# Optimization experiments

Hardware: AMD Instinct MI355X
Metric: run time of the kernel (lower is better)

The kernel has to match this reference:

```python
import jax, jax.numpy as jnp
import numpy as np

N = 100000   # nodes
E = 3200000  # edges (avg degree 32)
D = 128      # node_input_dim
H = 32       # hidden_dim
OUT = 3


def setup_inputs() -> dict:
    key = jax.random.key(0)
    ks = jax.random.split(key, 8)
    x = jax.random.normal(ks[0], (N, D), jnp.float32)
    edge_index = jax.random.randint(ks[1], (2, E), 0, N, dtype=jnp.int32)
    W1 = jax.random.normal(ks[2], (D, H), jnp.float32) * (1.0 / np.sqrt(D))
    b1 = jnp.zeros((H,), jnp.float32)
    W2 = jax.random.normal(ks[3], (H, H), jnp.float32) * (1.0 / np.sqrt(H))
    b2 = jnp.zeros((H,), jnp.float32)
    Wfc = jax.random.normal(ks[4], (H, OUT), jnp.float32) * (1.0 / np.sqrt(H))
    bfc = jnp.zeros((OUT,), jnp.float32)
    return {"x": x, "edge_index": edge_index, "W1": W1, "b1": b1,
            "W2": W2, "b2": b2, "Wfc": Wfc, "bfc": bfc}


def gcn_conv(x, W, b, src, dst, num_nodes):
    # PyG GCNConv defaults: transform, add self-loops, symmetric deg^-1/2 norm, bias.
    h = x @ W  # [N, H]
    ones = jnp.ones(src.shape[0], x.dtype)
    # degree with self-loop (+1), counted at target index (col) as in PyG
    deg = jax.ops.segment_sum(ones, dst, num_segments=num_nodes) + 1.0
    norm = jax.lax.rsqrt(deg)  # [N]
    coef = norm[src] * norm[dst]  # [E]
    msg = h[src] * coef[:, None]  # [E, H] gather + scale
    agg = jax.ops.segment_sum(msg, dst, num_segments=num_nodes)  # scatter-add
    # self-loop contribution: norm[i]^2 * h[i]
    agg = agg + h * (norm * norm)[:, None]
    return agg + b


def reference(x, edge_index, W1, b1, W2, b2, Wfc, bfc):
    src, dst = edge_index[0], edge_index[1]
    n = x.shape[0]
    h = jax.nn.relu(gcn_conv(x, W1, b1, src, dst, n))
    h = jax.nn.relu(gcn_conv(h, W2, b2, src, dst, n))
    return jax.nn.sigmoid(h @ Wfc + bfc)
```

## Files before the change

kernel.cpp:

```cpp
#include <hip/hip_runtime.h>
#include <hip/hip_fp16.h>
#include <math.h>

#define D_IN   128
#define H_DIM  32
#define OUT_DIM 3

#define BS      256
#define LOGBS   8
#define CAP_B   9088
#define EPB_P   8192
#define NB_MAX  1024

static __device__ inline unsigned int h2u(__half2 h) {
    union { __half2 h; unsigned int u; } c; c.h = h; return c.u;
}
static __device__ inline __half2 u2h(unsigned int u) {
    union { unsigned int u; __half2 h; } c; c.u = u; return c.h;
}
static __device__ inline __half2 sh2(__half2 v, int o) {
    return u2h((unsigned int)__shfl_xor((int)h2u(v), o));
}


__global__ void k_init_cur(int* bcur, int nb) {
    int i = blockIdx.x * blockDim.x + threadIdx.x;
    if (i < nb) bcur[i] = i * CAP_B;
}


__global__ __launch_bounds__(256) void k_part(
    const int* __restrict__ src, const int* __restrict__ dst,
    int* __restrict__ bcur, int* __restrict__ tmcsr, int e, int nb)
{
    __shared__ int hist[NB_MAX];
    __shared__ int cur[NB_MAX];
    const int t = threadIdx.x;
    for (int j = t; j < nb; j += 256) hist[j] = 0;
    __syncthreads();

    const int base = blockIdx.x * EPB_P;
    int d[EPB_P / 256], s[EPB_P / 256];
#pragma unroll
    for (int k = 0; k < EPB_P / 256; ++k) {
        int i = base + k * 256 + t;
        if (i < e) {
            d[k] = dst[i];
            s[k] = src[i];
            atomicAdd(&hist[d[k] >> LOGBS], 1);
        } else d[k] = -1;
    }
    __syncthreads();
    for (int j = t; j < nb; j += 256)
        cur[j] = hist[j] ? atomicAdd(&bcur[j], hist[j]) : 0;
    __syncthreads();
#pragma unroll
    for (int k = 0; k < EPB_P / 256; ++k) {
        if (d[k] >= 0) {
            int b = d[k] >> LOGBS;
            int pos = atomicAdd(&cur[b], 1);
            if (pos < (b + 1) * CAP_B)
                tmcsr[pos] = s[k] | ((d[k] & (BS - 1)) << 17);
        }
    }
}


__global__ __launch_bounds__(256) void k_build(
    int* __restrict__ tmcsr, const int* __restrict__ bcur,
    int* __restrict__ offs, int* __restrict__ ends, float* __restrict__ norm,
    int n)
{
    __shared__ int cnt[BS];
    __shared__ int ss[256];
    __shared__ int slice[CAP_B];

    const int t = threadIdx.x;
    const int b = blockIdx.x;
    const int bo = b * CAP_B;
    int m = bcur[b] - bo;
    if (m > CAP_B) m = CAP_B;

    cnt[t] = 0;
    __syncthreads();

    for (int i = t; i < m; i += 256)
        atomicAdd(&cnt[tmcsr[bo + i] >> 17], 1);
    __syncthreads();

    int c0 = cnt[t];
    ss[t] = c0;
    __syncthreads();
    for (int off = 1; off < 256; off <<= 1) {
        int u = (t >= off) ? ss[t - off] : 0;
        __syncthreads();
        ss[t] += u;
        __syncthreads();
    }
    int eb = ss[t] - c0;

    int node = (b << LOGBS) + t;
    if (node < n) {
        offs[node] = bo + eb;
        ends[node] = bo + eb + c0;
        norm[node] = rsqrtf((float)c0 + 1.0f);
    }
    cnt[t] = eb;
    __syncthreads();

    for (int i = t; i < m; i += 256) {
        int p = tmcsr[bo + i];
        int pos = atomicAdd(&cnt[p >> 17], 1);
        if (pos < CAP_B) slice[pos] = p & 0x1FFFF;
    }
    __syncthreads();

    for (int i = t; i < m; i += 256) tmcsr[bo + i] = slice[i];
}


__global__ __launch_bounds__(256) void k_gemm1(
    const float* __restrict__ x, const float* __restrict__ W1,
    const float* __restrict__ norm, __half* __restrict__ h1s, int n)
{
    __shared__ float Wl[D_IN * H_DIM];
    for (int i = threadIdx.x; i < D_IN * H_DIM; i += 256) Wl[i] = W1[i];
    __syncthreads();

    const int t = threadIdx.x;
    const int jg = t & 3;
    const int node = blockIdx.x * 64 + (t >> 2);
    if (node >= n) return;
    const int j0 = jg * 8;

    float acc[8];
#pragma unroll
    for (int j = 0; j < 8; ++j) acc[j] = 0.0f;

    const float* xrow = &x[(size_t)node * D_IN];
    for (int k = 0; k < D_IN; k += 4) {
        const float4 xv = *(const float4*)&xrow[k];
#pragma unroll
        for (int kk = 0; kk < 4; ++kk) {
            const float xs = (kk == 0) ? xv.x : (kk == 1) ? xv.y
                           : (kk == 2) ? xv.z : xv.w;
            const float4 wa = *(const float4*)&Wl[(k + kk) * H_DIM + j0];
            const float4 wb = *(const float4*)&Wl[(k + kk) * H_DIM + j0 + 4];
            acc[0] = fmaf(xs, wa.x, acc[0]);
            acc[1] = fmaf(xs, wa.y, acc[1]);
            acc[2] = fmaf(xs, wa.z, acc[2]);
            acc[3] = fmaf(xs, wa.w, acc[3]);
            acc[4] = fmaf(xs, wb.x, acc[4]);
            acc[5] = fmaf(xs, wb.y, acc[5]);
            acc[6] = fmaf(xs, wb.z, acc[6]);
            acc[7] = fmaf(xs, wb.w, acc[7]);
        }
    }

    const float nr = norm[node];
    uint4 pk;
    pk.x = h2u(__floats2half2_rn(acc[0]*nr, acc[1]*nr));
    pk.y = h2u(__floats2half2_rn(acc[2]*nr, acc[3]*nr));
    pk.z = h2u(__floats2half2_rn(acc[4]*nr, acc[5]*nr));
    pk.w = h2u(__floats2half2_rn(acc[6]*nr, acc[7]*nr));
    *(uint4*)&h1s[(size_t)node * H_DIM + j0] = pk;
}


__global__ __launch_bounds__(256) void k_gather_g2(
    const __half* __restrict__ hsA, const float* __restrict__ norm,
    const int* __restrict__ offs, const int* __restrict__ ends,
    const int* __restrict__ csr, const float* __restrict__ b1,
    const float* __restrict__ W2, __half* __restrict__ hsB, int n)
{
    __shared__ float Wl[H_DIM * 33];
    __shared__ float bl[H_DIM];
    for (int i = threadIdx.x; i < H_DIM * H_DIM; i += 256) {
        int k = i >> 5, j = i & 31;
        Wl[k * 33 + j] = W2[i];
    }
    if (threadIdx.x < H_DIM) bl[threadIdx.x] = b1[threadIdx.x];
    __syncthreads();

    const int t = threadIdx.x;
    const int node = blockIdx.x * 4 + (t >> 6);
    if (node >= n) return;
    const int lane = t & 63;
    const int g = lane >> 3;
    const int q = lane & 7;

    const int beg = offs[node];
    const int end = ends[node];
    const uint2* rows = (const uint2*)hsA;

    uint2 rs = rows[node * 8 + q];

    __half2 acc0 = u2h(0u), acc1 = u2h(0u);
    int j = beg + g;
    for (; j + 24 < end; j += 32) {
        int s0 = csr[j];
        int s1 = csr[j + 8];
        int s2 = csr[j + 16];
        int s3 = csr[j + 24];
        uint2 r0 = rows[s0 * 8 + q];
        uint2 r1 = rows[s1 * 8 + q];
        uint2 r2 = rows[s2 * 8 + q];
        uint2 r3 = rows[s3 * 8 + q];
        acc0 = __hadd2(acc0, __hadd2(__hadd2(u2h(r0.x), u2h(r1.x)),
                                     __hadd2(u2h(r2.x), u2h(r3.x))));
        acc1 = __hadd2(acc1, __hadd2(__hadd2(u2h(r0.y), u2h(r1.y)),
                                     __hadd2(u2h(r2.y), u2h(r3.y))));
    }
    for (; j < end; j += 8) {
        uint2 r0 = rows[csr[j] * 8 + q];
        acc0 = __hadd2(acc0, u2h(r0.x));
        acc1 = __hadd2(acc1, u2h(r0.y));
    }
    if (g == 0) {
        acc0 = __hadd2(acc0, u2h(rs.x));
        acc1 = __hadd2(acc1, u2h(rs.y));
    }

#pragma unroll
    for (int o = 8; o < 64; o <<= 1) {
        acc0 = __hadd2(acc0, sh2(acc0, o));
        acc1 = __hadd2(acc1, sh2(acc1, o));
    }

    const float nr = norm[node];
    float2 f0 = __half22float2(acc0);
    float2 f1 = __half22float2(acc1);
    const int kb = q * 4;
    float u0 = fmaxf(fmaf(f0.x, nr, bl[kb + 0]), 0.f);
    float u1 = fmaxf(fmaf(f0.y, nr, bl[kb + 1]), 0.f);
    float u2 = fmaxf(fmaf(f1.x, nr, bl[kb + 2]), 0.f);
    float u3 = fmaxf(fmaf(f1.y, nr, bl[kb + 3]), 0.f);

    float p[4];
#pragma unroll
    for (int jj = 0; jj < 4; ++jj) {
        int jc = g + 8 * jj;
        p[jj] = u0 * Wl[(kb + 0) * 33 + jc]
              + u1 * Wl[(kb + 1) * 33 + jc]
              + u2 * Wl[(kb + 2) * 33 + jc]
              + u3 * Wl[(kb + 3) * 33 + jc];
    }
#pragma unroll
    for (int o = 1; o < 8; o <<= 1) {
        p[0] += __shfl_xor(p[0], o); p[1] += __shfl_xor(p[1], o);
        p[2] += __shfl_xor(p[2], o); p[3] += __shfl_xor(p[3], o);
    }

    if (q == 0) {
        __half* rowB = &hsB[(size_t)node * H_DIM];
        rowB[g]      = __float2half(p[0] * nr);
        rowB[g + 8]  = __float2half(p[1] * nr);
        rowB[g + 16] = __float2half(p[2] * nr);
        rowB[g + 24] = __float2half(p[3] * nr);
    }
}


__global__ __launch_bounds__(256) void k_gather_fin(
    const __half* __restrict__ hs, const float* __restrict__ norm,
    const int* __restrict__ offs, const int* __restrict__ ends,
    const int* __restrict__ csr, const float* __restrict__ b2,
    const float* __restrict__ Wfc, const float* __restrict__ bfc,
    float* __restrict__ out, int n)
{
    const int t = threadIdx.x;
    const int node = blockIdx.x * 4 + (t >> 6);
    if (node >= n) return;
    const int lane = t & 63;
    const int g = lane >> 3;
    const int q = lane & 7;

    const int beg = offs[node];
    const int end = ends[node];
    const uint2* rows = (const uint2*)hs;

    uint2 rs = rows[node * 8 + q];

    __half2 acc0 = u2h(0u), acc1 = u2h(0u);
    int j = beg + g;
    for (; j + 24 < end; j += 32) {
        int s0 = csr[j];
        int s1 = csr[j + 8];
        int s2 = csr[j + 16];
        int s3 = csr[j + 24];
        uint2 r0 = rows[s0 * 8 + q];
        uint2 r1 = rows[s1 * 8 + q];
        uint2 r2 = rows[s2 * 8 + q];
        uint2 r3 = rows[s3 * 8 + q];
        acc0 = __hadd2(acc0, __hadd2(__hadd2(u2h(r0.x), u2h(r1.x)),
                                     __hadd2(u2h(r2.x), u2h(r3.x))));
        acc1 = __hadd2(acc1, __hadd2(__hadd2(u2h(r0.y), u2h(r1.y)),
                                     __hadd2(u2h(r2.y), u2h(r3.y))));
    }
    for (; j < end; j += 8) {
        uint2 r0 = rows[csr[j] * 8 + q];
        acc0 = __hadd2(acc0, u2h(r0.x));
        acc1 = __hadd2(acc1, u2h(r0.y));
    }
    if (g == 0) {
        acc0 = __hadd2(acc0, u2h(rs.x));
        acc1 = __hadd2(acc1, u2h(rs.y));
    }

#pragma unroll
    for (int o = 8; o < 64; o <<= 1) {
        acc0 = __hadd2(acc0, sh2(acc0, o));
        acc1 = __hadd2(acc1, sh2(acc1, o));
    }

    const float nr = norm[node];
    float2 f0 = __half22float2(acc0);
    float2 f1 = __half22float2(acc1);
    const int f = q * 4;
    float v0 = fmaxf(fmaf(f0.x, nr, b2[f + 0]), 0.f);
    float v1 = fmaxf(fmaf(f0.y, nr, b2[f + 1]), 0.f);
    float v2 = fmaxf(fmaf(f1.x, nr, b2[f + 2]), 0.f);
    float v3 = fmaxf(fmaf(f1.y, nr, b2[f + 3]), 0.f);
    float p0 = v0*Wfc[(f+0)*3+0] + v1*Wfc[(f+1)*3+0] + v2*Wfc[(f+2)*3+0] + v3*Wfc[(f+3)*3+0];
    float p1 = v0*Wfc[(f+0)*3+1] + v1*Wfc[(f+1)*3+1] + v2*Wfc[(f+2)*3+1] + v3*Wfc[(f+3)*3+1];
    float p2 = v0*Wfc[(f+0)*3+2] + v1*Wfc[(f+1)*3+2] + v2*Wfc[(f+2)*3+2] + v3*Wfc[(f+3)*3+2];
#pragma unroll
    for (int o = 1; o < 8; o <<= 1) {
        p0 += __shfl_xor(p0, o); p1 += __shfl_xor(p1, o); p2 += __shfl_xor(p2, o);
    }

    if (lane == 0) {
        out[(size_t)node * 3 + 0] = 1.0f / (1.0f + expf(-(p0 + bfc[0])));
        out[(size_t)node * 3 + 1] = 1.0f / (1.0f + expf(-(p1 + bfc[1])));
        out[(size_t)node * 3 + 2] = 1.0f / (1.0f + expf(-(p2 + bfc[2])));
    }
}


extern "C" void kernel_launch(void* const* d_in, const int* in_sizes, int n_in,
                              void* d_out, int out_size, void* d_ws, size_t ws_size,
                              hipStream_t stream)
{
    const float* x   = (const float*)d_in[0];
    const int*   ei  = (const int*)d_in[1];
    const float* W1  = (const float*)d_in[2];
    const float* b1  = (const float*)d_in[3];
    const float* W2  = (const float*)d_in[4];
    const float* b2  = (const float*)d_in[5];
    const float* Wfc = (const float*)d_in[6];
    const float* bfc = (const float*)d_in[7];
    float* out = (float*)d_out;

    const int n = in_sizes[0] / D_IN;
    const int e = in_sizes[1] / 2;
    const int* src = ei;
    const int* dst = ei + e;
    const int nb = (n + BS - 1) >> LOGBS;

    size_t nAl = ((size_t)n + 256) & ~(size_t)255;

    float* norm  = (float*)d_ws;
    int*   offs  = (int*)(norm + nAl);
    int*   ends  = offs + nAl;
    int*   bcur  = ends + nAl;
    int*   tmcsr = bcur + 1024;
    __half* HbA  = (__half*)(tmcsr + (size_t)nb * CAP_B);
    __half* HbB  = HbA + nAl * H_DIM;

    const int nb_gm = (n + 63) / 64;
    const int nb_p  = (e + EPB_P - 1) / EPB_P;
    const int nb_g  = (n + 3) / 4;

    k_init_cur<<<(nb + 255) / 256, 256, 0, stream>>>(bcur, nb);
    k_part <<<nb_p, 256, 0, stream>>>(src, dst, bcur, tmcsr, e, nb);
    k_build<<<nb, 256, 0, stream>>>(tmcsr, bcur, offs, ends, norm, n);

    k_gemm1<<<nb_gm, 256, 0, stream>>>(x, W1, norm, HbA, n);

    k_gather_g2<<<nb_g, 256, 0, stream>>>(HbA, norm, offs, ends, tmcsr,
                                          b1, W2, HbB, n);

    k_gather_fin<<<nb_g, 256, 0, stream>>>(HbB, norm, offs, ends, tmcsr,
                                           b2, Wfc, bfc, out, n);
}
```

Before: 208.8 us.

## Enlarge block sizes for partition, build, and GEMM kernels; coalesce layer-2 stores

Partitioning now uses 512 threads per block and handles 16384 edges per block. Bucket cursors become relative offsets, so the init kernel is replaced by a memset. The build and first-layer GEMM kernels move to 512 threads, with the GEMM covering 128 nodes per block. The layer-2 gather stages its outputs in shared memory and writes each half-precision row with 8-byte vector stores instead of scattered 2-byte writes. The aim is fewer launches, fewer partition blocks contending on global atomics, and more coalesced writes. In exchange, register pressure in the partition kernel rises, and the build kernel leaves half its threads idle during the scan.

```diff
diff --git a/kernel.cpp b/kernel.cpp
--- a/kernel.cpp
+++ b/kernel.cpp
@@ -9,7 +9,9 @@
 #define BS      256
 #define LOGBS   8
 #define CAP_B   9088
-#define EPB_P   8192
+#define TPB_P   512
+#define EPB_P   16384
+#define VPT_P   (EPB_P / TPB_P)
 #define NB_MAX  1024
 
 static __device__ inline unsigned int h2u(__half2 h) {
@@ -23,27 +25,21 @@
 }
 
 
-__global__ void k_init_cur(int* bcur, int nb) {
-    int i = blockIdx.x * blockDim.x + threadIdx.x;
-    if (i < nb) bcur[i] = i * CAP_B;
-}
-
-
-__global__ __launch_bounds__(256) void k_part(
+__global__ __launch_bounds__(TPB_P) void k_part(
     const int* __restrict__ src, const int* __restrict__ dst,
     int* __restrict__ bcur, int* __restrict__ tmcsr, int e, int nb)
 {
     __shared__ int hist[NB_MAX];
     __shared__ int cur[NB_MAX];
     const int t = threadIdx.x;
-    for (int j = t; j < nb; j += 256) hist[j] = 0;
+    for (int j = t; j < nb; j += TPB_P) hist[j] = 0;
     __syncthreads();
 
     const int base = blockIdx.x * EPB_P;
-    int d[EPB_P / 256], s[EPB_P / 256];
-#pragma unroll
-    for (int k = 0; k < EPB_P / 256; ++k) {
-        int i = base + k * 256 + t;
+    int d[VPT_P], s[VPT_P];
+#pragma unroll
+    for (int k = 0; k < VPT_P; ++k) {
+        int i = base + k * TPB_P + t;
         if (i < e) {
             d[k] = dst[i];
             s[k] = src[i];
@@ -51,85 +47,87 @@
         } else d[k] = -1;
     }
     __syncthreads();
-    for (int j = t; j < nb; j += 256)
+    for (int j = t; j < nb; j += TPB_P)
         cur[j] = hist[j] ? atomicAdd(&bcur[j], hist[j]) : 0;
     __syncthreads();
 #pragma unroll
-    for (int k = 0; k < EPB_P / 256; ++k) {
+    for (int k = 0; k < VPT_P; ++k) {
         if (d[k] >= 0) {
             int b = d[k] >> LOGBS;
             int pos = atomicAdd(&cur[b], 1);
-            if (pos < (b + 1) * CAP_B)
-                tmcsr[pos] = s[k] | ((d[k] & (BS - 1)) << 17);
+            if (pos < CAP_B)
+                tmcsr[b * CAP_B + pos] = s[k] | ((d[k] & (BS - 1)) << 17);
         }
     }
 }
 
 
-__global__ __launch_bounds__(256) void k_build(
+__global__ __launch_bounds__(512) void k_build(
     int* __restrict__ tmcsr, const int* __restrict__ bcur,
     int* __restrict__ offs, int* __restrict__ ends, float* __restrict__ norm,
     int n)
 {
     __shared__ int cnt[BS];
-    __shared__ int ss[256];
+    __shared__ int ss[BS];
     __shared__ int slice[CAP_B];
 
     const int t = threadIdx.x;
     const int b = blockIdx.x;
     const int bo = b * CAP_B;
-    int m = bcur[b] - bo;
+    int m = bcur[b];
     if (m > CAP_B) m = CAP_B;
 
-    cnt[t] = 0;
-    __syncthreads();
-
-    for (int i = t; i < m; i += 256)
+    if (t < BS) cnt[t] = 0;
+    __syncthreads();
+
+    for (int i = t; i < m; i += 512)
         atomicAdd(&cnt[tmcsr[bo + i] >> 17], 1);
     __syncthreads();
 
-    int c0 = cnt[t];
-    ss[t] = c0;
-    __syncthreads();
-    for (int off = 1; off < 256; off <<= 1) {
-        int u = (t >= off) ? ss[t - off] : 0;
+    int c0 = 0;
+    if (t < BS) { c0 = cnt[t]; ss[t] = c0; }
+    __syncthreads();
+    for (int off = 1; off < BS; off <<= 1) {
+        int u = 0;
+        if (t < BS && t >= off) u = ss[t - off];
         __syncthreads();
-        ss[t] += u;
+        if (t < BS) ss[t] += u;
         __syncthreads();
     }
-    int eb = ss[t] - c0;
-
-    int node = (b << LOGBS) + t;
-    if (node < n) {
-        offs[node] = bo + eb;
-        ends[node] = bo + eb + c0;
-        norm[node] = rsqrtf((float)c0 + 1.0f);
-    }
-    cnt[t] = eb;
-    __syncthreads();
-
-    for (int i = t; i < m; i += 256) {
+    if (t < BS) {
+        int eb = ss[t] - c0;
+        int node = (b << LOGBS) + t;
+        if (node < n) {
+            offs[node] = bo + eb;
+            ends[node] = bo + eb + c0;
+            norm[node] = rsqrtf((float)c0 + 1.0f);
+        }
+        cnt[t] = eb;
+    }
+    __syncthreads();
+
+    for (int i = t; i < m; i += 512) {
         int p = tmcsr[bo + i];
         int pos = atomicAdd(&cnt[p >> 17], 1);
         if (pos < CAP_B) slice[pos] = p & 0x1FFFF;
     }
     __syncthreads();
 
-    for (int i = t; i < m; i += 256) tmcsr[bo + i] = slice[i];
-}
-
-
-__global__ __launch_bounds__(256) void k_gemm1(
+    for (int i = t; i < m; i += 512) tmcsr[bo + i] = slice[i];
+}
+
+
+__global__ __launch_bounds__(512) void k_gemm1(
     const float* __restrict__ x, const float* __restrict__ W1,
     const float* __restrict__ norm, __half* __restrict__ h1s, int n)
 {
     __shared__ float Wl[D_IN * H_DIM];
-    for (int i = threadIdx.x; i < D_IN * H_DIM; i += 256) Wl[i] = W1[i];
+    for (int i = threadIdx.x; i < D_IN * H_DIM; i += 512) Wl[i] = W1[i];
     __syncthreads();
 
     const int t = threadIdx.x;
     const int jg = t & 3;
-    const int node = blockIdx.x * 64 + (t >> 2);
+    const int node = blockIdx.x * 128 + (t >> 2);
     if (node >= n) return;
     const int j0 = jg * 8;
 
@@ -175,6 +173,7 @@
 {
     __shared__ float Wl[H_DIM * 33];
     __shared__ float bl[H_DIM];
+    __shared__ float sout[4][33];
     for (int i = threadIdx.x; i < H_DIM * H_DIM; i += 256) {
         int k = i >> 5, j = i & 31;
         Wl[k * 33 + j] = W2[i];
@@ -183,7 +182,8 @@
     __syncthreads();
 
     const int t = threadIdx.x;
-    const int node = blockIdx.x * 4 + (t >> 6);
+    const int w = t >> 6;
+    const int node = blockIdx.x * 4 + w;
     if (node >= n) return;
     const int lane = t & 63;
     const int g = lane >> 3;
@@ -252,11 +252,17 @@
     }
 
     if (q == 0) {
-        __half* rowB = &hsB[(size_t)node * H_DIM];
-        rowB[g]      = __float2half(p[0] * nr);
-        rowB[g + 8]  = __float2half(p[1] * nr);
-        rowB[g + 16] = __float2half(p[2] * nr);
-        rowB[g + 24] = __float2half(p[3] * nr);
+        sout[w][g]      = p[0] * nr;
+        sout[w][g + 8]  = p[1] * nr;
+        sout[w][g + 16] = p[2] * nr;
+        sout[w][g + 24] = p[3] * nr;
+    }
+    if (lane < 8) {
+        float4 v = *(float4*)&sout[w][lane * 4];
+        uint2 wv;
+        wv.x = h2u(__floats2half2_rn(v.x, v.y));
+        wv.y = h2u(__floats2half2_rn(v.z, v.w));
+        ((uint2*)hsB)[node * 8 + lane] = wv;
     }
 }
 
@@ -367,15 +373,15 @@
     __half* HbA  = (__half*)(tmcsr + (size_t)nb * CAP_B);
     __half* HbB  = HbA + nAl * H_DIM;
 
-    const int nb_gm = (n + 63) / 64;
+    const int nb_gm = (n + 127) / 128;
     const int nb_p  = (e + EPB_P - 1) / EPB_P;
     const int nb_g  = (n + 3) / 4;
 
-    k_init_cur<<<(nb + 255) / 256, 256, 0, stream>>>(bcur, nb);
-    k_part <<<nb_p, 256, 0, stream>>>(src, dst, bcur, tmcsr, e, nb);
-    k_build<<<nb, 256, 0, stream>>>(tmcsr, bcur, offs, ends, norm, n);
-
-    k_gemm1<<<nb_gm, 256, 0, stream>>>(x, W1, norm, HbA, n);
+    hipMemsetAsync(bcur, 0, (size_t)nb * sizeof(int), stream);
+    k_part <<<nb_p, TPB_P, 0, stream>>>(src, dst, bcur, tmcsr, e, nb);
+    k_build<<<nb, 512, 0, stream>>>(tmcsr, bcur, offs, ends, norm, n);
+
+    k_gemm1<<<nb_gm, 512, 0, stream>>>(x, W1, norm, HbA, n);
 
     k_gather_g2<<<nb_g, 256, 0, stream>>>(HbA, norm, offs, ends, tmcsr,
                                           b1, W2, HbB, n);
```

Result: faster. 202.6 us (-3.0%).
